# Kernel optimization log

Measured on AMD Instinct MI355X. Metric: run time of the kernel, lower is better.

## Reference

```python
import math
import jax, jax.numpy as jnp
import numpy as np

IMG_SIZE = 2048
STRIDE = 8
NUM_CLASSES = 80
TOPK = 1000
CONF_THRESH = 0.05
NMS_THRESH = 0.6
CTR_CLAMP = 32.0
SCALE_CLAMP = math.log(1000.0 / 16)
ANCHOR_SIZES = np.array([[32,32],[64,32],[32,64],[64,64],[128,64],[64,128],[128,128],[256,128],[128,256]], dtype=np.float32)


def make_anchors():
    fmp = IMG_SIZE // STRIDE  # 256
    yy, xx = np.meshgrid(np.arange(fmp), np.arange(fmp), indexing='ij')
    xy = (np.stack([xx, yy], axis=-1).reshape(-1, 2).astype(np.float32) + 0.5) * STRIDE  # [fmp*fmp, 2]
    na = ANCHOR_SIZES.shape[0]
    xy = np.repeat(xy[:, None, :], na, axis=1)           # [fmp*fmp, na, 2]
    wh = np.tile(ANCHOR_SIZES[None, :, :], (fmp * fmp, 1, 1))  # [fmp*fmp, na, 2]
    return jnp.asarray(np.concatenate([xy, wh], axis=-1).reshape(-1, 4))  # [M, 4]


def setup_inputs() -> dict:
    key = jax.random.key(0)
    k1, k2 = jax.random.split(key)
    M = (IMG_SIZE // STRIDE) ** 2 * ANCHOR_SIZES.shape[0]
    cls_pred = jax.random.normal(k1, (M, NUM_CLASSES), dtype=jnp.float32) * 2.0 - 2.0
    reg_pred = jax.random.normal(k2, (M, 4), dtype=jnp.float32) * 0.5
    anchor_boxes = make_anchors()
    return {"cls_pred": cls_pred, "reg_pred": reg_pred, "anchor_boxes": anchor_boxes}


def decode_boxes(anchors, reg):
    # anchors, reg: [N, 4] (cx, cy, w, h) / (dx, dy, dw, dh)
    ctr_off = jnp.clip(reg[..., :2] * anchors[..., 2:], -CTR_CLAMP, CTR_CLAMP)
    ctr = anchors[..., :2] + ctr_off
    wh = anchors[..., 2:] * jnp.exp(jnp.minimum(reg[..., 2:], SCALE_CLAMP))
    return jnp.concatenate([ctr - 0.5 * wh, ctr + 0.5 * wh], axis=-1)


def iou_matrix(boxes):
    # boxes: [N, 4] x1y1x2y2 -> [N, N] IoU, matching the numpy NMS math
    x1, y1, x2, y2 = boxes[:, 0], boxes[:, 1], boxes[:, 2], boxes[:, 3]
    areas = (x2 - x1) * (y2 - y1)
    xx1 = jnp.maximum(x1[:, None], x1[None, :])
    yy1 = jnp.maximum(y1[:, None], y1[None, :])
    xx2 = jnp.minimum(x2[:, None], x2[None, :])
    yy2 = jnp.minimum(y2[:, None], y2[None, :])
    w = jnp.maximum(1e-10, xx2 - xx1)
    h = jnp.maximum(1e-10, yy2 - yy1)
    inter = w * h
    return inter / (areas[:, None] + areas[None, :] - inter + 1e-10)


def reference(cls_pred, reg_pred, anchor_boxes):
    # per-anchor best class score/label
    probs = jax.nn.sigmoid(cls_pred)                 # [M, C]
    scores_all = jnp.max(probs, axis=-1)             # [M]
    labels_all = jnp.argmax(probs, axis=-1)          # [M]
    # top-k filtering (scores sorted descending)
    scores, idx = jax.lax.top_k(scores_all, TOPK)    # [K]
    labels = labels_all[idx]
    reg = reg_pred[idx]
    anch = anchor_boxes[idx]
    # decode + normalize
    bboxes = jnp.clip(decode_boxes(anch, reg) / IMG_SIZE, 0.0, 1.0)  # [K, 4]
    valid = scores >= CONF_THRESH                    # conf filter as mask (fixed shape)
    # per-class greedy NMS: candidates are score-sorted, so greedy order = index order
    iou = iou_matrix(bboxes)                         # [K, K]
    same_cls = labels[:, None] == labels[None, :]    # [K, K]
    suppress_mat = (iou > NMS_THRESH) & same_cls     # j suppresses i if kept, same class, earlier
    idx_range = jnp.arange(TOPK)

    def body(i, keep):
        earlier_kept_overlap = jnp.any(keep & suppress_mat[:, i] & (idx_range < i))
        return keep.at[i].set(valid[i] & ~earlier_kept_overlap)

    keep = jax.lax.fori_loop(0, TOPK, body, jnp.zeros(TOPK, dtype=bool))
    return bboxes, scores, labels, keep
```

## Files before the change

kernel.cpp:

```cpp
#include <hip/hip_runtime.h>
#include <math.h>

#define M_ANCH   589824
#define NCLS     80
#define TOPK_N   1000
#define CAND_CAP 4096
#define NREP     16
#define NBIN     8192
#define KSHIFT   19

#define SCALE_CLAMP_F 4.135166556742356f
#define INV_IMG       (1.0f/2048.0f)

#define WS_H1R     0
#define WS_CNT     524288
#define WS_GBIN    524292
#define WS_MEMSET  524296
#define WS_CAND    524544
#define WS_BOXES   557312
#define WS_LABELS  573312
#define WS_VALID   577312
#define WS_SUP     581376
#define WS_MKEYS   709632

__device__ __forceinline__ unsigned fmap(unsigned b) {
    return (b & 0x80000000u) ? ~b : (b | 0x80000000u);
}
__device__ __forceinline__ unsigned funmap(unsigned k) {
    return (k & 0x80000000u) ? (k ^ 0x80000000u) : ~k;
}

__global__ __launch_bounds__(256) void k_rowmax(const float* __restrict__ cls,
                                                unsigned* __restrict__ mkeys,
                                                unsigned* __restrict__ h1r) {
    __shared__ unsigned lh[NBIN];
    int t = threadIdx.x;
    for (int b = t; b < NBIN; b += 256) lh[b] = 0;
    __syncthreads();
    int lane = t & 63, w = t >> 6;
    int part = lane & 3;
    int rsub = (w << 4) + (lane >> 2);
#pragma unroll
    for (int it = 0; it < 4; ++it) {
        int row = blockIdx.x * 256 + it * 64 + rsub;
        const float4* p = (const float4*)(cls + (size_t)row * NCLS) + part * 5;
        float m = -INFINITY;
#pragma unroll
        for (int i = 0; i < 5; ++i) {
            float4 v = p[i];
            m = fmaxf(m, fmaxf(fmaxf(v.x, v.y), fmaxf(v.z, v.w)));
        }
        m = fmaxf(m, __shfl_xor(m, 1));
        m = fmaxf(m, __shfl_xor(m, 2));
        if (part == 0) {
            unsigned key = fmap(__float_as_uint(m));
            mkeys[row] = key;
            atomicAdd(&lh[key >> KSHIFT], 1u);
        }
    }
    __syncthreads();
    unsigned rep = (blockIdx.x & (NREP - 1)) * NBIN;
    for (int b = t; b < NBIN; b += 256) {
        unsigned c = lh[b];
        if (c) atomicAdd(&h1r[rep + b], c);
    }
}

__global__ __launch_bounds__(1024) void k_find(const unsigned* __restrict__ h1r,
                                               unsigned* __restrict__ gbin) {
    __shared__ unsigned hist[NBIN];
    __shared__ unsigned csum[256];
    int t = threadIdx.x;
    for (int b = t; b < NBIN; b += 1024) {
        unsigned s = 0;
#pragma unroll
        for (int r = 0; r < NREP; ++r) s += h1r[r * NBIN + b];
        hist[b] = s;
    }
    __syncthreads();
    if (t < 256) {
        unsigned cs = 0;
        for (int k = 0; k < 32; ++k) cs += hist[t * 32 + k];
        csum[t] = cs;
    }
    __syncthreads();
    if (t == 0) {
        unsigned cum = 0, above = 0;
        int C = 0;
        for (int c = 255; c >= 0; --c) {
            if (cum + csum[c] >= TOPK_N || c == 0) { C = c; above = cum; break; }
            cum += csum[c];
        }
        int B = C * 32;
        unsigned cum2 = above;
        for (int b = C * 32 + 31; b >= C * 32; --b) {
            cum2 += hist[b];
            if (cum2 >= TOPK_N) { B = b; break; }
            if (b == C * 32) B = b;
        }
        *gbin = (B >= 1) ? (unsigned)(B - 1) : 0u;
    }
}

__global__ __launch_bounds__(256) void k_gather(const uint4* __restrict__ mk4,
                                                const unsigned* __restrict__ gbin,
                                                unsigned* __restrict__ cnt,
                                                unsigned long long* __restrict__ cand) {
    int tid = blockIdx.x * 256 + threadIdx.x;
    unsigned gb = *gbin;
    uint4 a = mk4[tid * 2];
    uint4 b4 = mk4[tid * 2 + 1];
    unsigned keys[8] = {a.x, a.y, a.z, a.w, b4.x, b4.y, b4.z, b4.w};
    int lc = 0;
    unsigned sel[8];
#pragma unroll
    for (int q = 0; q < 8; ++q)
        if ((keys[q] >> KSHIFT) >= gb) sel[lc++] = (unsigned)q;
    if (lc) {
        unsigned base = atomicAdd(cnt, (unsigned)lc);
        for (int q = 0; q < lc; ++q) {
            unsigned pos = base + (unsigned)q;
            if (pos < CAND_CAP) {
                unsigned i = (unsigned)tid * 8u + sel[q];
                float m = __uint_as_float(funmap(keys[sel[q]]));
                float e = (float)exp(-(double)m);
                float sc = 1.0f / (1.0f + e);
                cand[pos] = ((unsigned long long)__float_as_uint(sc) << 32)
                            | (unsigned)(~i);
            }
        }
    }
}

__global__ __launch_bounds__(256) void k_rank_decode(const unsigned* __restrict__ cnt,
                                                     const unsigned long long* __restrict__ cand,
                                                     const float* __restrict__ cls,
                                                     const float* __restrict__ reg,
                                                     const float* __restrict__ anch,
                                                     float* __restrict__ out,
                                                     float4* __restrict__ boxes_ws,
                                                     int* __restrict__ lab_ws,
                                                     int* __restrict__ val_ws) {
    __shared__ unsigned long long sh[CAND_CAP];
    int t = threadIdx.x;
    unsigned n = *cnt;
    if (n > CAND_CAP) n = CAND_CAP;
    for (int k = t; k < (int)n; k += 256) sh[k] = cand[k];
    __syncthreads();
    int k = blockIdx.x * 256 + t;
    if (k >= (int)n) return;
    unsigned long long key = sh[k];
    int rank = 0;
    for (int j = 0; j < (int)n; ++j) rank += (sh[j] > key) ? 1 : 0;
    if (rank >= TOPK_N) return;
    int r = rank;
    unsigned idx = ~(unsigned)(key & 0xFFFFFFFFull);
    float sc = __uint_as_float((unsigned)(key >> 32));
    const float* row = cls + (size_t)idx * NCLS;
    float best = -INFINITY;
    int lbl = 0;
    for (int c = 0; c < NCLS; ++c) {
        float v = row[c];
        if (v > best) { best = v; lbl = c; }
    }
    float4 rg = ((const float4*)reg)[idx];
    float4 an = ((const float4*)anch)[idx];
    float ox = fminf(fmaxf(rg.x * an.z, -32.0f), 32.0f);
    float oy = fminf(fmaxf(rg.y * an.w, -32.0f), 32.0f);
    float cx = an.x + ox, cy = an.y + oy;
    float w = an.z * expf(fminf(rg.z, SCALE_CLAMP_F));
    float h = an.w * expf(fminf(rg.w, SCALE_CLAMP_F));
    float x1 = fminf(fmaxf((cx - 0.5f * w) * INV_IMG, 0.0f), 1.0f);
    float y1 = fminf(fmaxf((cy - 0.5f * h) * INV_IMG, 0.0f), 1.0f);
    float x2 = fminf(fmaxf((cx + 0.5f * w) * INV_IMG, 0.0f), 1.0f);
    float y2 = fminf(fmaxf((cy + 0.5f * h) * INV_IMG, 0.0f), 1.0f);
    out[r * 4 + 0] = x1;
    out[r * 4 + 1] = y1;
    out[r * 4 + 2] = x2;
    out[r * 4 + 3] = y2;
    out[4 * TOPK_N + r] = sc;
    out[5 * TOPK_N + r] = (float)lbl;
    boxes_ws[r] = make_float4(x1, y1, x2, y2);
    lab_ws[r] = lbl;
    val_ws[r] = (sc >= 0.05f) ? 1 : 0;
}

__global__ __launch_bounds__(64) void k_sup(const float4* __restrict__ boxes,
                                            const int* __restrict__ labs,
                                            unsigned long long* __restrict__ sup) {
    int i = blockIdx.x;
    int lane = threadIdx.x;
    int cmax = i >> 6;
    float4 bi = boxes[i];
    float ai = (bi.z - bi.x) * (bi.w - bi.y);
    int li = labs[i];
    for (int c = 0; c <= cmax; ++c) {
        int j = c * 64 + lane;
        bool bit = false;
        if (j < TOPK_N) {
            float4 bj = boxes[j];
            float aj = (bj.z - bj.x) * (bj.w - bj.y);
            float xx1 = fmaxf(bi.x, bj.x), yy1 = fmaxf(bi.y, bj.y);
            float xx2 = fminf(bi.z, bj.z), yy2 = fminf(bi.w, bj.w);
            float w = fmaxf(1e-10f, xx2 - xx1);
            float h = fmaxf(1e-10f, yy2 - yy1);
            float inter = w * h;
            float iou = inter / (ai + aj - inter + 1e-10f);
            bit = (iou > 0.6f) && (labs[j] == li);
        }
        unsigned long long ball = __ballot(bit);
        if (lane == 0) sup[(size_t)i * 16 + c] = ball;
    }
}

__global__ __launch_bounds__(64) void k_nms(const unsigned long long* __restrict__ sup,
                                            const int* __restrict__ val,
                                            float* __restrict__ out_keep) {
    int lane = threadIdx.x;
    unsigned long long kw[16];
#pragma unroll
    for (int c = 0; c < 16; ++c) kw[c] = 0ull;
    unsigned long long lowmask = (lane == 0) ? 0ull : (~0ull >> (64 - lane));
    for (int c = 0; c < 16; ++c) {
        int b = c * 64 + lane;
        bool v = false;
        bool ext = false;
        unsigned long long m = 0ull;
        if (b < TOPK_N) {
            v = (val[b] != 0);
            const unsigned long long* rowp = sup + (size_t)b * 16;
            for (int w = 0; w < c; ++w) ext = ext || ((rowp[w] & kw[w]) != 0ull);
            m = rowp[c];
        }
        unsigned long long inchunk = m & lowmask;
        bool mykeep;
        if (__ballot(inchunk != 0ull) == 0ull) {
            mykeep = v && !ext;
        } else {
            mykeep = false;
            for (int i = 0; i < 64; ++i) {
                unsigned long long ball = __ballot(mykeep);
                if (lane == i) mykeep = v && !ext && ((ball & inchunk) == 0ull);
            }
        }
        unsigned long long ball2 = __ballot(mykeep);
        kw[c] = ball2;
        if (b < TOPK_N) out_keep[b] = ((ball2 >> lane) & 1ull) ? 1.0f : 0.0f;
    }
}

extern "C" void kernel_launch(void* const* d_in, const int* in_sizes, int n_in,
                              void* d_out, int out_size, void* d_ws, size_t ws_size,
                              hipStream_t stream) {
    const float* cls  = (const float*)d_in[0];
    const float* reg  = (const float*)d_in[1];
    const float* anch = (const float*)d_in[2];
    float* out = (float*)d_out;
    char* ws = (char*)d_ws;

    unsigned* h1r  = (unsigned*)(ws + WS_H1R);
    unsigned* cnt  = (unsigned*)(ws + WS_CNT);
    unsigned* gbin = (unsigned*)(ws + WS_GBIN);
    unsigned long long* cand = (unsigned long long*)(ws + WS_CAND);
    float4* boxes = (float4*)(ws + WS_BOXES);
    int* labs     = (int*)(ws + WS_LABELS);
    int* valid    = (int*)(ws + WS_VALID);
    unsigned long long* sup = (unsigned long long*)(ws + WS_SUP);
    unsigned* mkeys = (unsigned*)(ws + WS_MKEYS);

    hipMemsetAsync(ws, 0, WS_MEMSET, stream);

    k_rowmax<<<M_ANCH / 256, 256, 0, stream>>>(cls, mkeys, h1r);
    k_find  <<<1, 1024, 0, stream>>>(h1r, gbin);
    k_gather<<<M_ANCH / (256 * 8), 256, 0, stream>>>((const uint4*)mkeys, gbin, cnt, cand);
    k_rank_decode<<<CAND_CAP / 256, 256, 0, stream>>>(cnt, cand, cls, reg, anch,
                                                      out, boxes, labs, valid);
    k_sup   <<<TOPK_N, 64, 0, stream>>>(boxes, labs, sup);
    k_nms   <<<1, 64, 0, stream>>>(sup, valid, out + 6 * TOPK_N);
}
```

Measured before the change: 386.0 us.

## Fuse find/gather/rank/sup/nms into one last-block kernel; coalesce rowmax loads

Merges the threshold-find, candidate gather, rank+decode, suppression-matrix and NMS kernels into a single 144-block kernel. Every block redundantly rebuilds the histogram threshold, then compacts candidates with a block-wide prefix scan and one atomic per block. The last block to finish, detected through a done counter, does ranking, decode, IoU bitmask and NMS out of shared memory. k_rowmax now reads the class rows with fully coalesced float4 loads staged through LDS. This removes several launch gaps, but the serial tail now runs on one 1024-thread block, and each block repeats the 8192-bin histogram reduction.

```diff
diff --git a/kernel.cpp b/kernel.cpp
--- a/kernel.cpp
+++ b/kernel.cpp
@@ -8,20 +8,19 @@
 #define NREP     16
 #define NBIN     8192
 #define KSHIFT   19
+#define G2       144
+#define BT       1024
 
 #define SCALE_CLAMP_F 4.135166556742356f
 #define INV_IMG       (1.0f/2048.0f)
 
 #define WS_H1R     0
 #define WS_CNT     524288
-#define WS_GBIN    524292
+#define WS_DONE    524292
 #define WS_MEMSET  524296
 #define WS_CAND    524544
-#define WS_BOXES   557312
-#define WS_LABELS  573312
-#define WS_VALID   577312
-#define WS_SUP     581376
-#define WS_MKEYS   709632
+#define WS_SUP     557312
+#define WS_MKEYS   685568
 
 __device__ __forceinline__ unsigned fmap(unsigned b) {
     return (b & 0x80000000u) ? ~b : (b | 0x80000000u);
@@ -30,35 +29,35 @@
     return (k & 0x80000000u) ? (k ^ 0x80000000u) : ~k;
 }
 
-__global__ __launch_bounds__(256) void k_rowmax(const float* __restrict__ cls,
+__global__ __launch_bounds__(256) void k_rowmax(const float4* __restrict__ cls4,
                                                 unsigned* __restrict__ mkeys,
                                                 unsigned* __restrict__ h1r) {
     __shared__ unsigned lh[NBIN];
+    __shared__ float stage[1280];
     int t = threadIdx.x;
     for (int b = t; b < NBIN; b += 256) lh[b] = 0;
     __syncthreads();
-    int lane = t & 63, w = t >> 6;
-    int part = lane & 3;
-    int rsub = (w << 4) + (lane >> 2);
-#pragma unroll
-    for (int it = 0; it < 4; ++it) {
-        int row = blockIdx.x * 256 + it * 64 + rsub;
-        const float4* p = (const float4*)(cls + (size_t)row * NCLS) + part * 5;
+    int r = t >> 2, q = t & 3;
+    for (int ch = 0; ch < 4; ++ch) {
+        size_t base = (size_t)blockIdx.x * 5120 + (size_t)ch * 1280;
+#pragma unroll
+        for (int i = 0; i < 5; ++i) {
+            float4 v = cls4[base + i * 256 + t];
+            stage[i * 256 + t] = fmaxf(fmaxf(v.x, v.y), fmaxf(v.z, v.w));
+        }
+        __syncthreads();
         float m = -INFINITY;
 #pragma unroll
-        for (int i = 0; i < 5; ++i) {
-            float4 v = p[i];
-            m = fmaxf(m, fmaxf(fmaxf(v.x, v.y), fmaxf(v.z, v.w)));
-        }
+        for (int j = 0; j < 5; ++j) m = fmaxf(m, stage[r * 20 + q * 5 + j]);
         m = fmaxf(m, __shfl_xor(m, 1));
         m = fmaxf(m, __shfl_xor(m, 2));
-        if (part == 0) {
+        if (q == 0) {
             unsigned key = fmap(__float_as_uint(m));
-            mkeys[row] = key;
+            mkeys[blockIdx.x * 256 + ch * 64 + r] = key;
             atomicAdd(&lh[key >> KSHIFT], 1u);
         }
-    }
-    __syncthreads();
+        __syncthreads();
+    }
     unsigned rep = (blockIdx.x & (NREP - 1)) * NBIN;
     for (int b = t; b < NBIN; b += 256) {
         unsigned c = lh[b];
@@ -66,12 +65,26 @@
     }
 }
 
-__global__ __launch_bounds__(1024) void k_find(const unsigned* __restrict__ h1r,
-                                               unsigned* __restrict__ gbin) {
-    __shared__ unsigned hist[NBIN];
-    __shared__ unsigned csum[256];
+#define SM_BYTES 52768
+__global__ __launch_bounds__(1024) void k_mega(const uint4* __restrict__ mk4,
+                                               const float* __restrict__ cls,
+                                               const float4* __restrict__ reg4,
+                                               const float4* __restrict__ anch4,
+                                               const unsigned* __restrict__ h1r,
+                                               unsigned* __restrict__ cnt,
+                                               unsigned* __restrict__ done,
+                                               unsigned long long* __restrict__ cand_g,
+                                               unsigned long long* __restrict__ sup,
+                                               float* __restrict__ out) {
+    __shared__ __align__(16) char smraw[SM_BYTES];
+    __shared__ unsigned s_gbin, s_base, s_old;
+    __shared__ unsigned s_wsum[16];
     int t = threadIdx.x;
-    for (int b = t; b < NBIN; b += 1024) {
+    int lane = t & 63, wid = t >> 6;
+
+    unsigned* hist = (unsigned*)smraw;
+    unsigned* csum = (unsigned*)(smraw + 32768);
+    for (int b = t; b < NBIN; b += BT) {
         unsigned s = 0;
 #pragma unroll
         for (int r = 0; r < NREP; ++r) s += h1r[r * NBIN + b];
@@ -98,107 +111,109 @@
             if (cum2 >= TOPK_N) { B = b; break; }
             if (b == C * 32) B = b;
         }
-        *gbin = (B >= 1) ? (unsigned)(B - 1) : 0u;
-    }
-}
-
-__global__ __launch_bounds__(256) void k_gather(const uint4* __restrict__ mk4,
-                                                const unsigned* __restrict__ gbin,
-                                                unsigned* __restrict__ cnt,
-                                                unsigned long long* __restrict__ cand) {
-    int tid = blockIdx.x * 256 + threadIdx.x;
-    unsigned gb = *gbin;
-    uint4 a = mk4[tid * 2];
-    uint4 b4 = mk4[tid * 2 + 1];
-    unsigned keys[8] = {a.x, a.y, a.z, a.w, b4.x, b4.y, b4.z, b4.w};
-    int lc = 0;
-    unsigned sel[8];
-#pragma unroll
-    for (int q = 0; q < 8; ++q)
-        if ((keys[q] >> KSHIFT) >= gb) sel[lc++] = (unsigned)q;
-    if (lc) {
-        unsigned base = atomicAdd(cnt, (unsigned)lc);
-        for (int q = 0; q < lc; ++q) {
-            unsigned pos = base + (unsigned)q;
-            if (pos < CAND_CAP) {
-                unsigned i = (unsigned)tid * 8u + sel[q];
-                float m = __uint_as_float(funmap(keys[sel[q]]));
-                float e = (float)exp(-(double)m);
-                float sc = 1.0f / (1.0f + e);
-                cand[pos] = ((unsigned long long)__float_as_uint(sc) << 32)
-                            | (unsigned)(~i);
-            }
-        }
-    }
-}
-
-__global__ __launch_bounds__(256) void k_rank_decode(const unsigned* __restrict__ cnt,
-                                                     const unsigned long long* __restrict__ cand,
-                                                     const float* __restrict__ cls,
-                                                     const float* __restrict__ reg,
-                                                     const float* __restrict__ anch,
-                                                     float* __restrict__ out,
-                                                     float4* __restrict__ boxes_ws,
-                                                     int* __restrict__ lab_ws,
-                                                     int* __restrict__ val_ws) {
-    __shared__ unsigned long long sh[CAND_CAP];
-    int t = threadIdx.x;
-    unsigned n = *cnt;
+        s_gbin = (B >= 1) ? (unsigned)(B - 1) : 0u;
+    }
+    __syncthreads();
+    unsigned gb = s_gbin;
+
+    uint4 kv = mk4[blockIdx.x * BT + t];
+    unsigned keys[4] = {kv.x, kv.y, kv.z, kv.w};
+    unsigned lc = 0, selq[4];
+#pragma unroll
+    for (unsigned q = 0; q < 4; ++q)
+        if ((keys[q] >> KSHIFT) >= gb) selq[lc++] = q;
+    unsigned pre = lc;
+#pragma unroll
+    for (int d = 1; d < 64; d <<= 1) {
+        unsigned v = __shfl_up(pre, d);
+        if (lane >= d) pre += v;
+    }
+    if (lane == 63) s_wsum[wid] = pre;
+    unsigned mypre = pre - lc;
+    __syncthreads();
+    if (t == 0) {
+        unsigned s = 0;
+        for (int w = 0; w < 16; ++w) { unsigned v = s_wsum[w]; s_wsum[w] = s; s += v; }
+        s_base = s ? atomicAdd(cnt, s) : 0u;
+    }
+    __syncthreads();
+    unsigned base = s_base + s_wsum[wid] + mypre;
+    for (unsigned j = 0; j < lc; ++j) {
+        unsigned pos = base + j;
+        if (pos < CAND_CAP) {
+            unsigned q = selq[j];
+            unsigned i = ((unsigned)blockIdx.x * BT + (unsigned)t) * 4u + q;
+            float m = __uint_as_float(funmap(keys[q]));
+            float e = (float)exp(-(double)m);
+            float sc = 1.0f / (1.0f + e);
+            cand_g[pos] = ((unsigned long long)__float_as_uint(sc) << 32)
+                          | (unsigned)(~i);
+        }
+    }
+
+    __threadfence();
+    __syncthreads();
+    if (t == 0) s_old = atomicAdd(done, 1u);
+    __syncthreads();
+    if (s_old != G2 - 1) return;
+    __threadfence();
+
+    unsigned long long* sh_cand = (unsigned long long*)smraw;
+    float4* sh_box = (float4*)(smraw + 32768);
+    int*    sh_lab = (int*)(smraw + 48768);
+    unsigned n = atomicAdd(cnt, 0u);
     if (n > CAND_CAP) n = CAND_CAP;
-    for (int k = t; k < (int)n; k += 256) sh[k] = cand[k];
-    __syncthreads();
-    int k = blockIdx.x * 256 + t;
-    if (k >= (int)n) return;
-    unsigned long long key = sh[k];
-    int rank = 0;
-    for (int j = 0; j < (int)n; ++j) rank += (sh[j] > key) ? 1 : 0;
-    if (rank >= TOPK_N) return;
-    int r = rank;
-    unsigned idx = ~(unsigned)(key & 0xFFFFFFFFull);
-    float sc = __uint_as_float((unsigned)(key >> 32));
-    const float* row = cls + (size_t)idx * NCLS;
-    float best = -INFINITY;
-    int lbl = 0;
-    for (int c = 0; c < NCLS; ++c) {
-        float v = row[c];
-        if (v > best) { best = v; lbl = c; }
-    }
-    float4 rg = ((const float4*)reg)[idx];
-    float4 an = ((const float4*)anch)[idx];
-    float ox = fminf(fmaxf(rg.x * an.z, -32.0f), 32.0f);
-    float oy = fminf(fmaxf(rg.y * an.w, -32.0f), 32.0f);
-    float cx = an.x + ox, cy = an.y + oy;
-    float w = an.z * expf(fminf(rg.z, SCALE_CLAMP_F));
-    float h = an.w * expf(fminf(rg.w, SCALE_CLAMP_F));
-    float x1 = fminf(fmaxf((cx - 0.5f * w) * INV_IMG, 0.0f), 1.0f);
-    float y1 = fminf(fmaxf((cy - 0.5f * h) * INV_IMG, 0.0f), 1.0f);
-    float x2 = fminf(fmaxf((cx + 0.5f * w) * INV_IMG, 0.0f), 1.0f);
-    float y2 = fminf(fmaxf((cy + 0.5f * h) * INV_IMG, 0.0f), 1.0f);
-    out[r * 4 + 0] = x1;
-    out[r * 4 + 1] = y1;
-    out[r * 4 + 2] = x2;
-    out[r * 4 + 3] = y2;
-    out[4 * TOPK_N + r] = sc;
-    out[5 * TOPK_N + r] = (float)lbl;
-    boxes_ws[r] = make_float4(x1, y1, x2, y2);
-    lab_ws[r] = lbl;
-    val_ws[r] = (sc >= 0.05f) ? 1 : 0;
-}
-
-__global__ __launch_bounds__(64) void k_sup(const float4* __restrict__ boxes,
-                                            const int* __restrict__ labs,
-                                            unsigned long long* __restrict__ sup) {
-    int i = blockIdx.x;
-    int lane = threadIdx.x;
-    int cmax = i >> 6;
-    float4 bi = boxes[i];
-    float ai = (bi.z - bi.x) * (bi.w - bi.y);
-    int li = labs[i];
-    for (int c = 0; c <= cmax; ++c) {
-        int j = c * 64 + lane;
-        bool bit = false;
-        if (j < TOPK_N) {
-            float4 bj = boxes[j];
+    __syncthreads();
+    for (int k = t; k < (int)n; k += BT) sh_cand[k] = cand_g[k];
+    __syncthreads();
+
+    for (int k = t; k < (int)n; k += BT) {
+        unsigned long long key = sh_cand[k];
+        int rank = 0;
+        for (int j = 0; j < (int)n; ++j) rank += (sh_cand[j] > key) ? 1 : 0;
+        if (rank >= TOPK_N) continue;
+        int r = rank;
+        unsigned idx = ~(unsigned)(key & 0xFFFFFFFFull);
+        float sc = __uint_as_float((unsigned)(key >> 32));
+        const float* row = cls + (size_t)idx * NCLS;
+        float best = -INFINITY;
+        int lbl = 0;
+        for (int c = 0; c < NCLS; ++c) {
+            float v = row[c];
+            if (v > best) { best = v; lbl = c; }
+        }
+        float4 rg = reg4[idx];
+        float4 an = anch4[idx];
+        float ox = fminf(fmaxf(rg.x * an.z, -32.0f), 32.0f);
+        float oy = fminf(fmaxf(rg.y * an.w, -32.0f), 32.0f);
+        float cx = an.x + ox, cy = an.y + oy;
+        float w = an.z * expf(fminf(rg.z, SCALE_CLAMP_F));
+        float h = an.w * expf(fminf(rg.w, SCALE_CLAMP_F));
+        float x1 = fminf(fmaxf((cx - 0.5f * w) * INV_IMG, 0.0f), 1.0f);
+        float y1 = fminf(fmaxf((cy - 0.5f * h) * INV_IMG, 0.0f), 1.0f);
+        float x2 = fminf(fmaxf((cx + 0.5f * w) * INV_IMG, 0.0f), 1.0f);
+        float y2 = fminf(fmaxf((cy + 0.5f * h) * INV_IMG, 0.0f), 1.0f);
+        out[r * 4 + 0] = x1;
+        out[r * 4 + 1] = y1;
+        out[r * 4 + 2] = x2;
+        out[r * 4 + 3] = y2;
+        out[4 * TOPK_N + r] = sc;
+        out[5 * TOPK_N + r] = (float)lbl;
+        sh_box[r] = make_float4(x1, y1, x2, y2);
+        sh_lab[r] = lbl | ((sc >= 0.05f) ? 256 : 0);
+    }
+    __syncthreads();
+
+    for (int task = t; task < TOPK_N * 16; task += BT) {
+        int i = task >> 4, c = task & 15;
+        if (c > (i >> 6)) continue;
+        float4 bi = sh_box[i];
+        float ai = (bi.z - bi.x) * (bi.w - bi.y);
+        int li = sh_lab[i] & 0xFF;
+        unsigned long long word = 0ull;
+        int jmax = c * 64 + 64; if (jmax > TOPK_N) jmax = TOPK_N;
+        for (int j = c * 64; j < jmax; ++j) {
+            float4 bj = sh_box[j];
             float aj = (bj.z - bj.x) * (bj.w - bj.y);
             float xx1 = fmaxf(bi.x, bj.x), yy1 = fmaxf(bi.y, bj.y);
             float xx2 = fminf(bi.z, bj.z), yy2 = fminf(bi.w, bj.w);
@@ -206,46 +221,45 @@
             float h = fmaxf(1e-10f, yy2 - yy1);
             float inter = w * h;
             float iou = inter / (ai + aj - inter + 1e-10f);
-            bit = (iou > 0.6f) && (labs[j] == li);
-        }
-        unsigned long long ball = __ballot(bit);
-        if (lane == 0) sup[(size_t)i * 16 + c] = ball;
-    }
-}
-
-__global__ __launch_bounds__(64) void k_nms(const unsigned long long* __restrict__ sup,
-                                            const int* __restrict__ val,
-                                            float* __restrict__ out_keep) {
-    int lane = threadIdx.x;
-    unsigned long long kw[16];
-#pragma unroll
-    for (int c = 0; c < 16; ++c) kw[c] = 0ull;
-    unsigned long long lowmask = (lane == 0) ? 0ull : (~0ull >> (64 - lane));
-    for (int c = 0; c < 16; ++c) {
-        int b = c * 64 + lane;
-        bool v = false;
-        bool ext = false;
-        unsigned long long m = 0ull;
-        if (b < TOPK_N) {
-            v = (val[b] != 0);
-            const unsigned long long* rowp = sup + (size_t)b * 16;
-            for (int w = 0; w < c; ++w) ext = ext || ((rowp[w] & kw[w]) != 0ull);
-            m = rowp[c];
-        }
-        unsigned long long inchunk = m & lowmask;
-        bool mykeep;
-        if (__ballot(inchunk != 0ull) == 0ull) {
-            mykeep = v && !ext;
-        } else {
-            mykeep = false;
-            for (int i = 0; i < 64; ++i) {
-                unsigned long long ball = __ballot(mykeep);
-                if (lane == i) mykeep = v && !ext && ((ball & inchunk) == 0ull);
+            if ((iou > 0.6f) && ((sh_lab[j] & 0xFF) == li))
+                word |= (1ull << (j & 63));
+        }
+        sup[(size_t)i * 16 + c] = word;
+    }
+    __syncthreads();
+
+    if (t < 64) {
+        unsigned long long kw[16];
+#pragma unroll
+        for (int c = 0; c < 16; ++c) kw[c] = 0ull;
+        unsigned long long lowmask = (lane == 0) ? 0ull : (~0ull >> (64 - lane));
+        for (int c = 0; c < 16; ++c) {
+            int b = c * 64 + lane;
+            bool v = false;
+            bool ext = false;
+            unsigned long long m = 0ull;
+            if (b < TOPK_N) {
+                v = ((sh_lab[b] >> 8) & 1) != 0;
+                const unsigned long long* rowp = sup + (size_t)b * 16;
+                for (int w = 0; w < c; ++w) ext = ext || ((rowp[w] & kw[w]) != 0ull);
+                m = rowp[c];
             }
-        }
-        unsigned long long ball2 = __ballot(mykeep);
-        kw[c] = ball2;
-        if (b < TOPK_N) out_keep[b] = ((ball2 >> lane) & 1ull) ? 1.0f : 0.0f;
+            unsigned long long inchunk = m & lowmask;
+            bool mykeep;
+            if (__ballot(inchunk != 0ull) == 0ull) {
+                mykeep = v && !ext;
+            } else {
+                mykeep = false;
+                for (int i = 0; i < 64; ++i) {
+                    unsigned long long ball = __ballot(mykeep);
+                    if (lane == i) mykeep = v && !ext && ((ball & inchunk) == 0ull);
+                }
+            }
+            unsigned long long ball2 = __ballot(mykeep);
+            kw[c] = ball2;
+            if (b < TOPK_N)
+                out[6 * TOPK_N + b] = ((ball2 >> lane) & 1ull) ? 1.0f : 0.0f;
+        }
     }
 }
 
@@ -260,21 +274,15 @@
 
     unsigned* h1r  = (unsigned*)(ws + WS_H1R);
     unsigned* cnt  = (unsigned*)(ws + WS_CNT);
-    unsigned* gbin = (unsigned*)(ws + WS_GBIN);
+    unsigned* done = (unsigned*)(ws + WS_DONE);
     unsigned long long* cand = (unsigned long long*)(ws + WS_CAND);
-    float4* boxes = (float4*)(ws + WS_BOXES);
-    int* labs     = (int*)(ws + WS_LABELS);
-    int* valid    = (int*)(ws + WS_VALID);
-    unsigned long long* sup = (unsigned long long*)(ws + WS_SUP);
+    unsigned long long* sup  = (unsigned long long*)(ws + WS_SUP);
     unsigned* mkeys = (unsigned*)(ws + WS_MKEYS);
 
     hipMemsetAsync(ws, 0, WS_MEMSET, stream);
 
-    k_rowmax<<<M_ANCH / 256, 256, 0, stream>>>(cls, mkeys, h1r);
-    k_find  <<<1, 1024, 0, stream>>>(h1r, gbin);
-    k_gather<<<M_ANCH / (256 * 8), 256, 0, stream>>>((const uint4*)mkeys, gbin, cnt, cand);
-    k_rank_decode<<<CAND_CAP / 256, 256, 0, stream>>>(cnt, cand, cls, reg, anch,
-                                                      out, boxes, labs, valid);
-    k_sup   <<<TOPK_N, 64, 0, stream>>>(boxes, labs, sup);
-    k_nms   <<<1, 64, 0, stream>>>(sup, valid, out + 6 * TOPK_N);
-}
+    k_rowmax<<<M_ANCH / 256, 256, 0, stream>>>((const float4*)cls, mkeys, h1r);
+    k_mega  <<<G2, BT, 0, stream>>>((const uint4*)mkeys, cls,
+                                    (const float4*)reg, (const float4*)anch,
+                                    h1r, cnt, done, cand, sup, out);
+}
```

New measurement: 748.3 us. +93.9%, slower.
